# Optimization experiments

Measured on AMD Instinct MI355X. Metric: run time of the kernel, lower is better.

## Reference

```python
import jax, jax.numpy as jnp
import numpy as np

D_MODEL = 1024
H = 16
D_K = D_MODEL // H
NEG = -1000000000.0


def setup_inputs() -> dict:
    key = jax.random.key(0)
    ks = jax.random.split(key, 12)
    B, S, D = 2, 2048, D_MODEL
    scale = 1.0 / np.sqrt(D)
    inp = {
        "q": jax.random.normal(ks[0], (B, S, D), jnp.float32),
        "k": jax.random.normal(ks[1], (B, S, D), jnp.float32),
        "v": jax.random.normal(ks[2], (B, S, D), jnp.float32),
        "mask": jnp.tril(jnp.ones((S, S), bool))[None, None],  # causal (1,1,S,S)
        "Wq": jax.random.normal(ks[3], (D, D), jnp.float32) * scale,
        "bq": jax.random.normal(ks[4], (D,), jnp.float32) * scale,
        "Wk": jax.random.normal(ks[5], (D, D), jnp.float32) * scale,
        "bk": jax.random.normal(ks[6], (D,), jnp.float32) * scale,
        "Wv": jax.random.normal(ks[7], (D, D), jnp.float32) * scale,
        "bv": jax.random.normal(ks[8], (D,), jnp.float32) * scale,
        "Wo": jax.random.normal(ks[9], (D, D), jnp.float32) * scale,
        "bo": jax.random.normal(ks[10], (D,), jnp.float32) * scale,
    }
    return inp


def _split_heads(x):
    B, S, _ = x.shape
    return x.reshape(B, S, H, D_K).transpose(0, 2, 1, 3)  # (B,H,S,dk)


def reference(q, k, v, mask, Wq, bq, Wk, bk, Wv, bv, Wo, bo):
    # nn.Linear: x @ W.T + b
    query = _split_heads(q @ Wq.T + bq)
    key_ = _split_heads(k @ Wk.T + bk)
    value = _split_heads(v @ Wv.T + bv)
    scores = jnp.einsum("bhqd,bhkd->bhqk", query, key_) / jnp.sqrt(
        jnp.asarray(D_K, jnp.float32)
    )
    scores = jnp.where(mask, scores, NEG)  # masked_fill(mask==0, -1e9)
    attn = jax.nn.softmax(scores, axis=-1)  # dropout p=0 -> identity
    x = jnp.einsum("bhqk,bhkd->bhqd", attn, value)
    B, _, S, _ = x.shape
    x = x.transpose(0, 2, 1, 3).reshape(B, S, D_MODEL)
    return x @ Wo.T + bo
```

## Files before the change

kernel.cpp:

```cpp
#include <hip/hip_runtime.h>
#include <stdint.h>

typedef unsigned short ushort_t;
typedef __attribute__((ext_vector_type(8))) __bf16 bf16x8;
typedef __attribute__((ext_vector_type(4))) float f32x4;
typedef __attribute__((ext_vector_type(4))) unsigned int uint32x4;

__device__ __forceinline__ ushort_t f2bf(float f) {
  unsigned u = __float_as_uint(f);
  u += 0x7FFFu + ((u >> 16) & 1u);
  return (ushort_t)(u >> 16);
}

__device__ __forceinline__ uint32x4 ld8_f32(const float* p) {
  f32x4 a = *(const f32x4*)p;
  f32x4 b = *(const f32x4*)(p + 4);
  uint32x4 r;
  r.x = (unsigned)f2bf(a[0]) | ((unsigned)f2bf(a[1]) << 16);
  r.y = (unsigned)f2bf(a[2]) | ((unsigned)f2bf(a[3]) << 16);
  r.z = (unsigned)f2bf(b[0]) | ((unsigned)f2bf(b[1]) << 16);
  r.w = (unsigned)f2bf(b[2]) | ((unsigned)f2bf(b[3]) << 16);
  return r;
}
__device__ __forceinline__ uint32x4 ld8_bf16(const ushort_t* p) {
  return *(const uint32x4*)p;
}

__device__ __forceinline__ void gll16(const void* g, void* l) {
  __builtin_amdgcn_global_load_lds((const __attribute__((address_space(1))) void*)g,
                                   (__attribute__((address_space(3))) void*)l,
                                   16, 0, 0);
}

struct CvtArgs {
  const float* src[7];
  ushort_t* dst[7];
  int cnt[7];
};
__global__ void cvt_multi(CvtArgs a) {
  const int seg = blockIdx.y;
  const int idx = (blockIdx.x * 256 + threadIdx.x) * 8;
  if (idx < a.cnt[seg])
    *(uint32x4*)(a.dst[seg] + idx) = ld8_f32(a.src[seg] + idx);
}

__device__ __forceinline__ void gemm_tile_lds(const ushort_t* __restrict__ Ablk,
                                              const ushort_t* __restrict__ Wblk,
                                              ushort_t* As, ushort_t* Bs,
                                              const int K, const int w, const int l,
                                              f32x4 acc[4][4])
{
  const int sr = l >> 2;
  const int sk = (l & 3) << 3;
  const int lr = l & 15;
  const int q4 = l >> 4;
  const int wrow = (w >> 1) << 6;
  const int wcol = (w & 1) << 6;

  for (int k0 = 0; k0 < K; k0 += 32) {
#pragma unroll
    for (int cc = 0; cc < 2; ++cc) {
      const int ch  = cc * 4 + w;
      const int row = ch * 16 + sr;
      gll16(Ablk + (size_t)row * K + k0 + sk, As + ch * 512 + l * 8);
      gll16(Wblk + (size_t)row * K + k0 + sk, Bs + ch * 512 + l * 8);
    }
    __syncthreads();
    bf16x8 a[4], b[4];
#pragma unroll
    for (int i = 0; i < 4; ++i)
      a[i] = *(const bf16x8*)(As + (wrow + i * 16 + lr) * 32 + q4 * 8);
#pragma unroll
    for (int j = 0; j < 4; ++j)
      b[j] = *(const bf16x8*)(Bs + (wcol + j * 16 + lr) * 32 + q4 * 8);
#pragma unroll
    for (int i = 0; i < 4; ++i)
#pragma unroll
      for (int j = 0; j < 4; ++j)
        acc[i][j] = __builtin_amdgcn_mfma_f32_16x16x32_bf16(a[i], b[j], acc[i][j], 0, 0, 0);
    __syncthreads();
  }
}

template<bool A_F32, bool B_F32>
__device__ __forceinline__ void gemm_tile_reg(const void* __restrict__ Ablk_,
                                              const void* __restrict__ Wblk_,
                                              ushort_t* As, ushort_t* Bs,
                                              const int K, const int w, const int l,
                                              f32x4 acc[4][4])
{
  const float*    Af = (const float*)Ablk_;
  const ushort_t* Ab = (const ushort_t*)Ablk_;
  const float*    Wf = (const float*)Wblk_;
  const ushort_t* Wb = (const ushort_t*)Wblk_;
  const int sr = l >> 2, sk = (l & 3) << 3;
  const int lr = l & 15, q4 = l >> 4;
  const int wrow = (w >> 1) << 6, wcol = (w & 1) << 6;

  for (int k0 = 0; k0 < K; k0 += 32) {
    uint32x4 ra[2], rb[2];
#pragma unroll
    for (int cc = 0; cc < 2; ++cc) {
      const int ch  = cc * 4 + w;
      const int row = ch * 16 + sr;
      ra[cc] = A_F32 ? ld8_f32(Af + (size_t)row * K + k0 + sk)
                     : ld8_bf16(Ab + (size_t)row * K + k0 + sk);
      rb[cc] = B_F32 ? ld8_f32(Wf + (size_t)row * K + k0 + sk)
                     : ld8_bf16(Wb + (size_t)row * K + k0 + sk);
    }
    __syncthreads();
#pragma unroll
    for (int cc = 0; cc < 2; ++cc) {
      const int ch = cc * 4 + w;
      *(uint32x4*)(As + ch * 512 + l * 8) = ra[cc];
      *(uint32x4*)(Bs + ch * 512 + l * 8) = rb[cc];
    }
    __syncthreads();
    bf16x8 a[4], b[4];
#pragma unroll
    for (int i = 0; i < 4; ++i)
      a[i] = *(const bf16x8*)(As + (wrow + i * 16 + lr) * 32 + q4 * 8);
#pragma unroll
    for (int j = 0; j < 4; ++j)
      b[j] = *(const bf16x8*)(Bs + (wcol + j * 16 + lr) * 32 + q4 * 8);
#pragma unroll
    for (int i = 0; i < 4; ++i)
#pragma unroll
      for (int j = 0; j < 4; ++j)
        acc[i][j] = __builtin_amdgcn_mfma_f32_16x16x32_bf16(a[i], b[j], acc[i][j], 0, 0, 0);
  }
}

__device__ __forceinline__ void proj_epilogue(int z, f32x4 acc[4][4], const float* bias,
                                              ushort_t* O, int bm, int bn, int w, int l)
{
  const int lr = l & 15, q4 = l >> 4;
  const int wrow = (w >> 1) << 6, wcol = (w & 1) << 6;
  if (z == 2) {
#pragma unroll
    for (int i = 0; i < 4; ++i) {
      const int r0 = bm * 128 + wrow + i * 16 + q4 * 4;
      const int b_ = r0 >> 11, s_ = r0 & 2047;
#pragma unroll
      for (int j = 0; j < 4; ++j) {
        const int c = bn * 128 + wcol + j * 16 + lr;
        const float bb = bias[c];
        const int hb = b_ * 16 + (c >> 6);
        const int d_ = c & 63;
        ushort4 pk;
        pk.x = f2bf(acc[i][j][0] + bb);
        pk.y = f2bf(acc[i][j][1] + bb);
        pk.z = f2bf(acc[i][j][2] + bb);
        pk.w = f2bf(acc[i][j][3] + bb);
        *(ushort4*)(O + ((size_t)hb * 64 + d_) * 2048 + s_) = pk;
      }
    }
  } else {
#pragma unroll
    for (int i = 0; i < 4; ++i) {
#pragma unroll
      for (int j = 0; j < 4; ++j) {
        const int c = bn * 128 + wcol + j * 16 + lr;
        const float bb = bias[c];
        const int h_ = c >> 6, d_ = c & 63;
#pragma unroll
        for (int rg = 0; rg < 4; ++rg) {
          const int r = bm * 128 + wrow + i * 16 + q4 * 4 + rg;
          const int b_ = r >> 11, s_ = r & 2047;
          O[((size_t)(b_ * 16 + h_) * 2048 + s_) * 64 + d_] = f2bf(acc[i][j][rg] + bb);
        }
      }
    }
  }
}

__device__ __forceinline__ void out_epilogue(f32x4 acc[4][4], const float* bo,
                                             float* out, int bm, int bn, int w, int l)
{
  const int lr = l & 15, q4 = l >> 4;
  const int wrow = (w >> 1) << 6, wcol = (w & 1) << 6;
#pragma unroll
  for (int i = 0; i < 4; ++i) {
#pragma unroll
    for (int j = 0; j < 4; ++j) {
      const int c = bn * 128 + wcol + j * 16 + lr;
      const float bb = bo[c];
#pragma unroll
      for (int rg = 0; rg < 4; ++rg) {
        const int r = bm * 128 + wrow + i * 16 + q4 * 4 + rg;
        out[(size_t)r * 1024 + c] = acc[i][j][rg] + bb;
      }
    }
  }
}

__launch_bounds__(256, 2)
__global__ void proj_qkv_bf16(const ushort_t* __restrict__ qb, const ushort_t* __restrict__ kb,
                              const ushort_t* __restrict__ vb,
                              const ushort_t* __restrict__ Wqb, const ushort_t* __restrict__ Wkb,
                              const ushort_t* __restrict__ Wvb,
                              const float* __restrict__ bq, const float* __restrict__ bk,
                              const float* __restrict__ bv,
                              ushort_t* __restrict__ Qo, ushort_t* __restrict__ Ko,
                              ushort_t* __restrict__ Vo)
{
  const int z = blockIdx.z;
  const ushort_t* A = (z == 0) ? qb : (z == 1) ? kb : vb;
  const ushort_t* W = (z == 0) ? Wqb : (z == 1) ? Wkb : Wvb;
  const float* bias = (z == 0) ? bq : (z == 1) ? bk : bv;
  ushort_t* O       = (z == 0) ? Qo : (z == 1) ? Ko : Vo;

  const int K = 1024;
  const int bm = blockIdx.y, bn = blockIdx.x;
  const int t = threadIdx.x, w = t >> 6, l = t & 63;
  __shared__ ushort_t As[128 * 32];
  __shared__ ushort_t Bs[128 * 32];
  f32x4 acc[4][4];
#pragma unroll
  for (int i = 0; i < 4; ++i)
#pragma unroll
    for (int j = 0; j < 4; ++j) acc[i][j] = (f32x4)0.0f;
  gemm_tile_lds(A + (size_t)(bm * 128) * K, W + (size_t)(bn * 128) * K, As, Bs, K, w, l, acc);
  proj_epilogue(z, acc, bias, O, bm, bn, w, l);
}

__launch_bounds__(256, 2)
__global__ void proj_qkv_f32(const float* __restrict__ qi, const float* __restrict__ ki,
                             const float* __restrict__ vi,
                             const float* __restrict__ Wq, const float* __restrict__ Wk,
                             const float* __restrict__ Wv,
                             const float* __restrict__ bq, const float* __restrict__ bk,
                             const float* __restrict__ bv,
                             ushort_t* __restrict__ Qo, ushort_t* __restrict__ Ko,
                             ushort_t* __restrict__ Vo)
{
  const int z = blockIdx.z;
  const float* A    = (z == 0) ? qi : (z == 1) ? ki : vi;
  const float* W    = (z == 0) ? Wq : (z == 1) ? Wk : Wv;
  const float* bias = (z == 0) ? bq : (z == 1) ? bk : bv;
  ushort_t* O       = (z == 0) ? Qo : (z == 1) ? Ko : Vo;
  const int K = 1024;
  const int bm = blockIdx.y, bn = blockIdx.x;
  const int t = threadIdx.x, w = t >> 6, l = t & 63;
  __shared__ ushort_t As[128 * 32];
  __shared__ ushort_t Bs[128 * 32];
  f32x4 acc[4][4];
#pragma unroll
  for (int i = 0; i < 4; ++i)
#pragma unroll
    for (int j = 0; j < 4; ++j) acc[i][j] = (f32x4)0.0f;
  gemm_tile_reg<true, true>(A + (size_t)(bm * 128) * K, W + (size_t)(bn * 128) * K,
                            As, Bs, K, w, l, acc);
  proj_epilogue(z, acc, bias, O, bm, bn, w, l);
}

#define PPAD 72
__device__ __forceinline__ void attn_phase(const ushort_t* __restrict__ Qbase,
                                           const ushort_t* __restrict__ Kbase,
                                           const ushort_t* __restrict__ Vbase,
                                           ushort_t* __restrict__ X,
                                           int q0, int hb, int w, int l,
                                           ushort_t* Ks, ushort_t* Vt, ushort_t* Ps)
{
  const int S = 2048;
  const int lr = l & 15, q4 = l >> 4;

  bf16x8 qa[2][2];
#pragma unroll
  for (int ks = 0; ks < 2; ++ks)
#pragma unroll
    for (int mf = 0; mf < 2; ++mf)
      qa[ks][mf] = *(const bf16x8*)(Qbase + (size_t)(q0 + w * 32 + mf * 16 + lr) * 64
                                    + ks * 32 + q4 * 8);

  f32x4 o_acc[2][4];
  float lsum[2][4];
#pragma unroll
  for (int i = 0; i < 2; ++i)
#pragma unroll
    for (int j = 0; j < 4; ++j) o_acc[i][j] = (f32x4)0.0f;
#pragma unroll
  for (int i = 0; i < 2; ++i)
#pragma unroll
    for (int rg = 0; rg < 4; ++rg) lsum[i][rg] = 0.0f;

  const int nkt = (q0 >> 6) + 2;
  const int diag0 = q0 >> 6;
  const int strow = l >> 3;
  const int stcol = (l & 7) * 8;

  uint32x4 kreg[2], vreg[2];
#pragma unroll
  for (int cc = 0; cc < 2; ++cc) {
    const int ch = cc * 4 + w;
    const int row = ch * 8 + strow;
    kreg[cc] = *(const uint32x4*)(Kbase + (size_t)row * 64 + stcol);
    vreg[cc] = *(const uint32x4*)(Vbase + (size_t)row * S + stcol);
  }

  for (int kt = 0; kt < nkt; ++kt) {
    __syncthreads();
#pragma unroll
    for (int cc = 0; cc < 2; ++cc) {
      const int ch = cc * 4 + w;
      const int row = ch * 8 + strow;
      *(uint32x4*)(Ks + row * PPAD + stcol) = kreg[cc];
      *(uint32x4*)(Vt + row * PPAD + stcol) = vreg[cc];
    }
    __syncthreads();

    const int ktn = (kt + 1 < nkt) ? kt + 1 : kt;
#pragma unroll
    for (int cc = 0; cc < 2; ++cc) {
      const int ch = cc * 4 + w;
      const int row = ch * 8 + strow;
      kreg[cc] = *(const uint32x4*)(Kbase + (size_t)(ktn * 64 + row) * 64 + stcol);
      vreg[cc] = *(const uint32x4*)(Vbase + (size_t)row * S + ktn * 64 + stcol);
    }

    f32x4 s_acc[2][4];
#pragma unroll
    for (int i = 0; i < 2; ++i)
#pragma unroll
      for (int j = 0; j < 4; ++j) s_acc[i][j] = (f32x4)0.0f;
#pragma unroll
    for (int ks = 0; ks < 2; ++ks)
#pragma unroll
      for (int nf = 0; nf < 4; ++nf) {
        bf16x8 kb = *(const bf16x8*)(Ks + (nf * 16 + lr) * PPAD + ks * 32 + q4 * 8);
#pragma unroll
        for (int mf = 0; mf < 2; ++mf)
          s_acc[mf][nf] = __builtin_amdgcn_mfma_f32_16x16x32_bf16(qa[ks][mf], kb,
                                                                  s_acc[mf][nf], 0, 0, 0);
      }

    const bool need_mask = (kt >= diag0);
#pragma unroll
    for (int mf = 0; mf < 2; ++mf) {
#pragma unroll
      for (int rg = 0; rg < 4; ++rg) {
        const int qi = q0 + w * 32 + mf * 16 + q4 * 4 + rg;
#pragma unroll
        for (int nf = 0; nf < 4; ++nf) {
          const int kvi = kt * 64 + nf * 16 + lr;
          const float x = __builtin_fmaf(s_acc[mf][nf][rg], 0.125f, -12.0f);
          float p = __expf(x);
          if (need_mask && kvi > qi) p = 0.0f;
          s_acc[mf][nf][rg] = p;
          lsum[mf][rg] += p;
        }
      }
    }

    ushort_t* Pw = Ps + w * (32 * PPAD);
#pragma unroll
    for (int mf = 0; mf < 2; ++mf)
#pragma unroll
      for (int nf = 0; nf < 4; ++nf)
#pragma unroll
        for (int rg = 0; rg < 4; ++rg)
          Pw[(mf * 16 + q4 * 4 + rg) * PPAD + nf * 16 + lr] = f2bf(s_acc[mf][nf][rg]);

    __syncthreads();

#pragma unroll
    for (int ks = 0; ks < 2; ++ks) {
      bf16x8 pa[2];
#pragma unroll
      for (int mf = 0; mf < 2; ++mf)
        pa[mf] = *(const bf16x8*)(Pw + (mf * 16 + lr) * PPAD + ks * 32 + q4 * 8);
#pragma unroll
      for (int df = 0; df < 4; ++df) {
        bf16x8 vb = *(const bf16x8*)(Vt + (df * 16 + lr) * PPAD + ks * 32 + q4 * 8);
#pragma unroll
        for (int mf = 0; mf < 2; ++mf)
          o_acc[mf][df] = __builtin_amdgcn_mfma_f32_16x16x32_bf16(pa[mf], vb,
                                                                 o_acc[mf][df], 0, 0, 0);
      }
    }
  }

  const int b_ = hb >> 4, h_ = hb & 15;
#pragma unroll
  for (int mf = 0; mf < 2; ++mf) {
#pragma unroll
    for (int rg = 0; rg < 4; ++rg) {
      float s = lsum[mf][rg];
      s += __shfl_xor(s, 1);
      s += __shfl_xor(s, 2);
      s += __shfl_xor(s, 4);
      s += __shfl_xor(s, 8);
      const float inv = 1.0f / s;
      const int r = q0 + w * 32 + mf * 16 + q4 * 4 + rg;
#pragma unroll
      for (int df = 0; df < 4; ++df) {
        const int c = h_ * 64 + df * 16 + lr;
        X[((size_t)b_ * 2048 + r) * 1024 + c] = f2bf(o_acc[mf][df][rg] * inv);
      }
    }
  }
}

__launch_bounds__(256)
__global__ void attn(const ushort_t* __restrict__ Qh, const ushort_t* __restrict__ Kh,
                     const ushort_t* __restrict__ Vh, ushort_t* __restrict__ X)
{
  const int S = 2048;
  const int pair = blockIdx.x;
  const int hb = blockIdx.y;

  __shared__ ushort_t Ks[64 * PPAD];
  __shared__ ushort_t Vt[64 * PPAD];
  __shared__ ushort_t Ps[4 * 32 * PPAD];

  const int t = threadIdx.x, w = t >> 6, l = t & 63;
  const ushort_t* Qbase = Qh + (size_t)hb * S * 64;
  const ushort_t* Kbase = Kh + (size_t)hb * S * 64;
  const ushort_t* Vbase = Vh + (size_t)hb * 64 * S;

  attn_phase(Qbase, Kbase, Vbase, X, pair * 128, hb, w, l, Ks, Vt, Ps);
  attn_phase(Qbase, Kbase, Vbase, X, (15 - pair) * 128, hb, w, l, Ks, Vt, Ps);
}

__launch_bounds__(256, 2)
__global__ void out_gemm_bf16(const ushort_t* __restrict__ Xin, const ushort_t* __restrict__ Wob,
                              const float* __restrict__ bo, float* __restrict__ out)
{
  const int K = 1024;
  const int bm = blockIdx.y, bn = blockIdx.x;
  const int t = threadIdx.x, w = t >> 6, l = t & 63;
  __shared__ ushort_t As[128 * 32];
  __shared__ ushort_t Bs[128 * 32];
  f32x4 acc[4][4];
#pragma unroll
  for (int i = 0; i < 4; ++i)
#pragma unroll
    for (int j = 0; j < 4; ++j) acc[i][j] = (f32x4)0.0f;
  gemm_tile_lds(Xin + (size_t)(bm * 128) * K, Wob + (size_t)(bn * 128) * K,
                As, Bs, K, w, l, acc);
  out_epilogue(acc, bo, out, bm, bn, w, l);
}

__launch_bounds__(256, 2)
__global__ void out_gemm_f32(const ushort_t* __restrict__ Xin, const float* __restrict__ Wo,
                             const float* __restrict__ bo, float* __restrict__ out)
{
  const int K = 1024;
  const int bm = blockIdx.y, bn = blockIdx.x;
  const int t = threadIdx.x, w = t >> 6, l = t & 63;
  __shared__ ushort_t As[128 * 32];
  __shared__ ushort_t Bs[128 * 32];
  f32x4 acc[4][4];
#pragma unroll
  for (int i = 0; i < 4; ++i)
#pragma unroll
    for (int j = 0; j < 4; ++j) acc[i][j] = (f32x4)0.0f;
  gemm_tile_reg<false, true>(Xin + (size_t)(bm * 128) * K, Wo + (size_t)(bn * 128) * K,
                             As, Bs, K, w, l, acc);
  out_epilogue(acc, bo, out, bm, bn, w, l);
}

extern "C" void kernel_launch(void* const* d_in, const int* in_sizes, int n_in,
                              void* d_out, int out_size, void* d_ws, size_t ws_size,
                              hipStream_t stream) {
  (void)in_sizes; (void)n_in; (void)out_size;
  const float* q  = (const float*)d_in[0];
  const float* k  = (const float*)d_in[1];
  const float* v  = (const float*)d_in[2];
  const float* Wq = (const float*)d_in[4];
  const float* bq = (const float*)d_in[5];
  const float* Wk = (const float*)d_in[6];
  const float* bk = (const float*)d_in[7];
  const float* Wv = (const float*)d_in[8];
  const float* bv = (const float*)d_in[9];
  const float* Wo = (const float*)d_in[10];
  const float* bo = (const float*)d_in[11];

  ushort_t* ws = (ushort_t*)d_ws;
  const size_t SEG = (size_t)2 * 2048 * 1024;
  const size_t WSEG = (size_t)1024 * 1024;
  const size_t NEED = (3 * SEG + 4 * WSEG + 2 * SEG) * sizeof(ushort_t);

  if (ws_size >= NEED) {
    ushort_t* qb  = ws;
    ushort_t* kb  = qb + SEG;
    ushort_t* vb  = kb + SEG;
    ushort_t* Wqb = vb + SEG;
    ushort_t* Wkb = Wqb + WSEG;
    ushort_t* Wvb = Wkb + WSEG;
    ushort_t* Wob = Wvb + WSEG;
    ushort_t* Qh  = Wob + WSEG;
    ushort_t* Kh  = Qh + SEG;
    ushort_t* X   = qb;
    ushort_t* Vh  = (ushort_t*)d_out;

    CvtArgs ca;
    ca.src[0] = q;  ca.dst[0] = qb;  ca.cnt[0] = (int)SEG;
    ca.src[1] = k;  ca.dst[1] = kb;  ca.cnt[1] = (int)SEG;
    ca.src[2] = v;  ca.dst[2] = vb;  ca.cnt[2] = (int)SEG;
    ca.src[3] = Wq; ca.dst[3] = Wqb; ca.cnt[3] = (int)WSEG;
    ca.src[4] = Wk; ca.dst[4] = Wkb; ca.cnt[4] = (int)WSEG;
    ca.src[5] = Wv; ca.dst[5] = Wvb; ca.cnt[5] = (int)WSEG;
    ca.src[6] = Wo; ca.dst[6] = Wob; ca.cnt[6] = (int)WSEG;
    cvt_multi<<<dim3(2048, 7), 256, 0, stream>>>(ca);

    proj_qkv_bf16<<<dim3(8, 32, 3), 256, 0, stream>>>(qb, kb, vb, Wqb, Wkb, Wvb,
                                                      bq, bk, bv, Qh, Kh, Vh);
    attn<<<dim3(8, 32), 256, 0, stream>>>(Qh, Kh, Vh, X);
    out_gemm_bf16<<<dim3(8, 32), 256, 0, stream>>>(X, Wob, bo, (float*)d_out);
  } else {
    ushort_t* Qh = ws;
    ushort_t* Kh = Qh + SEG;
    ushort_t* X  = Kh + SEG;
    ushort_t* Vh = (ushort_t*)d_out;
    proj_qkv_f32<<<dim3(8, 32, 3), 256, 0, stream>>>(q, k, v, Wq, Wk, Wv,
                                                     bq, bk, bv, Qh, Kh, Vh);
    attn<<<dim3(8, 32), 256, 0, stream>>>(Qh, Kh, Vh, X);
    out_gemm_f32<<<dim3(8, 32), 256, 0, stream>>>(X, Wo, bo, (float*)d_out);
  }
}
```

Before: 244.8 us.

## Split attention into 64-row query tiles with heavy-first scheduling

Replaces the two-phase 128-row paired causal attention block with one block per 64-row query tile, launching 1024 blocks ordered longest-first and interleaving heads across blocks. Each wave handles 16 query rows, which cuts registers and shared memory so four blocks can fit per CU. The barrier before the P·V step becomes a wave-local LDS wait, since each wave only reads its own P rows. The cost is that every K/V tile is loaded and staged twice as often per head, and load balance now depends on the hardware dispatching blocks in launch order.

Result: faster. 231.6 us (-5.4%).

```diff
diff --git a/kernel.cpp b/kernel.cpp
--- a/kernel.cpp
+++ b/kernel.cpp
@@ -255,171 +255,129 @@
 }
 
 #define PPAD 72
-__device__ __forceinline__ void attn_phase(const ushort_t* __restrict__ Qbase,
-                                           const ushort_t* __restrict__ Kbase,
-                                           const ushort_t* __restrict__ Vbase,
-                                           ushort_t* __restrict__ X,
-                                           int q0, int hb, int w, int l,
-                                           ushort_t* Ks, ushort_t* Vt, ushort_t* Ps)
-{
-  const int S = 2048;
-  const int lr = l & 15, q4 = l >> 4;
-
-  bf16x8 qa[2][2];
-#pragma unroll
-  for (int ks = 0; ks < 2; ++ks)
-#pragma unroll
-    for (int mf = 0; mf < 2; ++mf)
-      qa[ks][mf] = *(const bf16x8*)(Qbase + (size_t)(q0 + w * 32 + mf * 16 + lr) * 64
-                                    + ks * 32 + q4 * 8);
-
-  f32x4 o_acc[2][4];
-  float lsum[2][4];
-#pragma unroll
-  for (int i = 0; i < 2; ++i)
-#pragma unroll
-    for (int j = 0; j < 4; ++j) o_acc[i][j] = (f32x4)0.0f;
-#pragma unroll
-  for (int i = 0; i < 2; ++i)
-#pragma unroll
-    for (int rg = 0; rg < 4; ++rg) lsum[i][rg] = 0.0f;
-
-  const int nkt = (q0 >> 6) + 2;
-  const int diag0 = q0 >> 6;
-  const int strow = l >> 3;
-  const int stcol = (l & 7) * 8;
-
-  uint32x4 kreg[2], vreg[2];
-#pragma unroll
-  for (int cc = 0; cc < 2; ++cc) {
-    const int ch = cc * 4 + w;
-    const int row = ch * 8 + strow;
-    kreg[cc] = *(const uint32x4*)(Kbase + (size_t)row * 64 + stcol);
-    vreg[cc] = *(const uint32x4*)(Vbase + (size_t)row * S + stcol);
-  }
-
-  for (int kt = 0; kt < nkt; ++kt) {
-    __syncthreads();
-#pragma unroll
-    for (int cc = 0; cc < 2; ++cc) {
-      const int ch = cc * 4 + w;
-      const int row = ch * 8 + strow;
-      *(uint32x4*)(Ks + row * PPAD + stcol) = kreg[cc];
-      *(uint32x4*)(Vt + row * PPAD + stcol) = vreg[cc];
-    }
-    __syncthreads();
-
-    const int ktn = (kt + 1 < nkt) ? kt + 1 : kt;
-#pragma unroll
-    for (int cc = 0; cc < 2; ++cc) {
-      const int ch = cc * 4 + w;
-      const int row = ch * 8 + strow;
-      kreg[cc] = *(const uint32x4*)(Kbase + (size_t)(ktn * 64 + row) * 64 + stcol);
-      vreg[cc] = *(const uint32x4*)(Vbase + (size_t)row * S + ktn * 64 + stcol);
-    }
-
-    f32x4 s_acc[2][4];
-#pragma unroll
-    for (int i = 0; i < 2; ++i)
-#pragma unroll
-      for (int j = 0; j < 4; ++j) s_acc[i][j] = (f32x4)0.0f;
-#pragma unroll
-    for (int ks = 0; ks < 2; ++ks)
-#pragma unroll
-      for (int nf = 0; nf < 4; ++nf) {
-        bf16x8 kb = *(const bf16x8*)(Ks + (nf * 16 + lr) * PPAD + ks * 32 + q4 * 8);
-#pragma unroll
-        for (int mf = 0; mf < 2; ++mf)
-          s_acc[mf][nf] = __builtin_amdgcn_mfma_f32_16x16x32_bf16(qa[ks][mf], kb,
-                                                                  s_acc[mf][nf], 0, 0, 0);
-      }
-
-    const bool need_mask = (kt >= diag0);
-#pragma unroll
-    for (int mf = 0; mf < 2; ++mf) {
-#pragma unroll
-      for (int rg = 0; rg < 4; ++rg) {
-        const int qi = q0 + w * 32 + mf * 16 + q4 * 4 + rg;
-#pragma unroll
-        for (int nf = 0; nf < 4; ++nf) {
-          const int kvi = kt * 64 + nf * 16 + lr;
-          const float x = __builtin_fmaf(s_acc[mf][nf][rg], 0.125f, -12.0f);
-          float p = __expf(x);
-          if (need_mask && kvi > qi) p = 0.0f;
-          s_acc[mf][nf][rg] = p;
-          lsum[mf][rg] += p;
-        }
-      }
-    }
-
-    ushort_t* Pw = Ps + w * (32 * PPAD);
-#pragma unroll
-    for (int mf = 0; mf < 2; ++mf)
-#pragma unroll
-      for (int nf = 0; nf < 4; ++nf)
-#pragma unroll
-        for (int rg = 0; rg < 4; ++rg)
-          Pw[(mf * 16 + q4 * 4 + rg) * PPAD + nf * 16 + lr] = f2bf(s_acc[mf][nf][rg]);
-
-    __syncthreads();
-
-#pragma unroll
-    for (int ks = 0; ks < 2; ++ks) {
-      bf16x8 pa[2];
-#pragma unroll
-      for (int mf = 0; mf < 2; ++mf)
-        pa[mf] = *(const bf16x8*)(Pw + (mf * 16 + lr) * PPAD + ks * 32 + q4 * 8);
-#pragma unroll
-      for (int df = 0; df < 4; ++df) {
-        bf16x8 vb = *(const bf16x8*)(Vt + (df * 16 + lr) * PPAD + ks * 32 + q4 * 8);
-#pragma unroll
-        for (int mf = 0; mf < 2; ++mf)
-          o_acc[mf][df] = __builtin_amdgcn_mfma_f32_16x16x32_bf16(pa[mf], vb,
-                                                                 o_acc[mf][df], 0, 0, 0);
-      }
-    }
-  }
-
-  const int b_ = hb >> 4, h_ = hb & 15;
-#pragma unroll
-  for (int mf = 0; mf < 2; ++mf) {
-#pragma unroll
-    for (int rg = 0; rg < 4; ++rg) {
-      float s = lsum[mf][rg];
-      s += __shfl_xor(s, 1);
-      s += __shfl_xor(s, 2);
-      s += __shfl_xor(s, 4);
-      s += __shfl_xor(s, 8);
-      const float inv = 1.0f / s;
-      const int r = q0 + w * 32 + mf * 16 + q4 * 4 + rg;
-#pragma unroll
-      for (int df = 0; df < 4; ++df) {
-        const int c = h_ * 64 + df * 16 + lr;
-        X[((size_t)b_ * 2048 + r) * 1024 + c] = f2bf(o_acc[mf][df][rg] * inv);
-      }
-    }
-  }
-}
-
-__launch_bounds__(256)
+__launch_bounds__(256, 4)
 __global__ void attn(const ushort_t* __restrict__ Qh, const ushort_t* __restrict__ Kh,
                      const ushort_t* __restrict__ Vh, ushort_t* __restrict__ X)
 {
   const int S = 2048;
-  const int pair = blockIdx.x;
-  const int hb = blockIdx.y;
+  const int id = blockIdx.x;
+  const int hb = (id & 7) * 4 + ((id >> 3) & 3);
+  const int qt = 31 - (id >> 5);
+  const int q0 = qt * 64;
 
   __shared__ ushort_t Ks[64 * PPAD];
   __shared__ ushort_t Vt[64 * PPAD];
-  __shared__ ushort_t Ps[4 * 32 * PPAD];
+  __shared__ ushort_t Ps[4 * 16 * PPAD];
 
   const int t = threadIdx.x, w = t >> 6, l = t & 63;
+  const int lr = l & 15, q4 = l >> 4;
+
   const ushort_t* Qbase = Qh + (size_t)hb * S * 64;
   const ushort_t* Kbase = Kh + (size_t)hb * S * 64;
   const ushort_t* Vbase = Vh + (size_t)hb * 64 * S;
 
-  attn_phase(Qbase, Kbase, Vbase, X, pair * 128, hb, w, l, Ks, Vt, Ps);
-  attn_phase(Qbase, Kbase, Vbase, X, (15 - pair) * 128, hb, w, l, Ks, Vt, Ps);
+  bf16x8 qa[2];
+#pragma unroll
+  for (int ks = 0; ks < 2; ++ks)
+    qa[ks] = *(const bf16x8*)(Qbase + (size_t)(q0 + w * 16 + lr) * 64 + ks * 32 + q4 * 8);
+
+  f32x4 o_acc[4];
+  float lsum[4];
+#pragma unroll
+  for (int j = 0; j < 4; ++j) { o_acc[j] = (f32x4)0.0f; lsum[j] = 0.0f; }
+
+  const int nkt = qt + 1;
+  const int strow = l >> 3;
+  const int stcol = (l & 7) * 8;
+
+  uint32x4 kreg[2], vreg[2];
+#pragma unroll
+  for (int cc = 0; cc < 2; ++cc) {
+    const int row = (cc * 4 + w) * 8 + strow;
+    kreg[cc] = *(const uint32x4*)(Kbase + (size_t)row * 64 + stcol);
+    vreg[cc] = *(const uint32x4*)(Vbase + (size_t)row * S + stcol);
+  }
+
+  for (int kt = 0; kt < nkt; ++kt) {
+    __syncthreads();
+#pragma unroll
+    for (int cc = 0; cc < 2; ++cc) {
+      const int row = (cc * 4 + w) * 8 + strow;
+      *(uint32x4*)(Ks + row * PPAD + stcol) = kreg[cc];
+      *(uint32x4*)(Vt + row * PPAD + stcol) = vreg[cc];
+    }
+    __syncthreads();
+
+    const int ktn = (kt + 1 < nkt) ? kt + 1 : kt;
+#pragma unroll
+    for (int cc = 0; cc < 2; ++cc) {
+      const int row = (cc * 4 + w) * 8 + strow;
+      kreg[cc] = *(const uint32x4*)(Kbase + (size_t)(ktn * 64 + row) * 64 + stcol);
+      vreg[cc] = *(const uint32x4*)(Vbase + (size_t)row * S + ktn * 64 + stcol);
+    }
+
+    f32x4 s_acc[4];
+#pragma unroll
+    for (int j = 0; j < 4; ++j) s_acc[j] = (f32x4)0.0f;
+#pragma unroll
+    for (int ks = 0; ks < 2; ++ks)
+#pragma unroll
+      for (int nf = 0; nf < 4; ++nf) {
+        bf16x8 kb = *(const bf16x8*)(Ks + (nf * 16 + lr) * PPAD + ks * 32 + q4 * 8);
+        s_acc[nf] = __builtin_amdgcn_mfma_f32_16x16x32_bf16(qa[ks], kb, s_acc[nf], 0, 0, 0);
+      }
+
+    const bool need_mask = (kt == qt);
+#pragma unroll
+    for (int rg = 0; rg < 4; ++rg) {
+      const int qi = q0 + w * 16 + q4 * 4 + rg;
+#pragma unroll
+      for (int nf = 0; nf < 4; ++nf) {
+        const int kvi = kt * 64 + nf * 16 + lr;
+        const float x = __builtin_fmaf(s_acc[nf][rg], 0.125f, -12.0f);
+        float p = __expf(x);
+        if (need_mask && kvi > qi) p = 0.0f;
+        s_acc[nf][rg] = p;
+        lsum[rg] += p;
+      }
+    }
+
+    ushort_t* Pw = Ps + w * (16 * PPAD);
+#pragma unroll
+    for (int nf = 0; nf < 4; ++nf)
+#pragma unroll
+      for (int rg = 0; rg < 4; ++rg)
+        Pw[(q4 * 4 + rg) * PPAD + nf * 16 + lr] = f2bf(s_acc[nf][rg]);
+
+    __asm__ volatile("s_waitcnt lgkmcnt(0)" ::: "memory");
+
+#pragma unroll
+    for (int ks = 0; ks < 2; ++ks) {
+      bf16x8 pa = *(const bf16x8*)(Pw + lr * PPAD + ks * 32 + q4 * 8);
+#pragma unroll
+      for (int df = 0; df < 4; ++df) {
+        bf16x8 vb = *(const bf16x8*)(Vt + (df * 16 + lr) * PPAD + ks * 32 + q4 * 8);
+        o_acc[df] = __builtin_amdgcn_mfma_f32_16x16x32_bf16(pa, vb, o_acc[df], 0, 0, 0);
+      }
+    }
+  }
+
+  const int b_ = hb >> 4, h_ = hb & 15;
+#pragma unroll
+  for (int rg = 0; rg < 4; ++rg) {
+    float s = lsum[rg];
+    s += __shfl_xor(s, 1);
+    s += __shfl_xor(s, 2);
+    s += __shfl_xor(s, 4);
+    s += __shfl_xor(s, 8);
+    const float inv = 1.0f / s;
+    const int r = q0 + w * 16 + q4 * 4 + rg;
+#pragma unroll
+    for (int df = 0; df < 4; ++df) {
+      const int c = h_ * 64 + df * 16 + lr;
+      X[((size_t)b_ * 2048 + r) * 1024 + c] = f2bf(o_acc[df][rg] * inv);
+    }
+  }
 }
 
 __launch_bounds__(256, 2)
@@ -506,7 +464,7 @@
 
     proj_qkv_bf16<<<dim3(8, 32, 3), 256, 0, stream>>>(qb, kb, vb, Wqb, Wkb, Wvb,
                                                       bq, bk, bv, Qh, Kh, Vh);
-    attn<<<dim3(8, 32), 256, 0, stream>>>(Qh, Kh, Vh, X);
+    attn<<<dim3(1024), 256, 0, stream>>>(Qh, Kh, Vh, X);
     out_gemm_bf16<<<dim3(8, 32), 256, 0, stream>>>(X, Wob, bo, (float*)d_out);
   } else {
     ushort_t* Qh = ws;
@@ -515,7 +473,7 @@
     ushort_t* Vh = (ushort_t*)d_out;
     proj_qkv_f32<<<dim3(8, 32, 3), 256, 0, stream>>>(q, k, v, Wq, Wk, Wv,
                                                      bq, bk, bv, Qh, Kh, Vh);
-    attn<<<dim3(8, 32), 256, 0, stream>>>(Qh, Kh, Vh, X);
+    attn<<<dim3(1024), 256, 0, stream>>>(Qh, Kh, Vh, X);
     out_gemm_f32<<<dim3(8, 32), 256, 0, stream>>>(X, Wo, bo, (float*)d_out);
   }
 }
```
